# Optimization experiments

Measured on AMD Instinct MI355X. Metric: run time of the kernel, lower is better.

## Reference

```python
import jax, jax.numpy as jnp
import numpy as np

D_MODEL = 1024
N_HEADS = 16
D_HEAD = D_MODEL // N_HEADS


def setup_inputs() -> dict:
    key = jax.random.key(0)
    ks = jax.random.split(key, 5)
    scale = 1.0 / np.sqrt(D_MODEL)
    return {
        "x": jax.random.normal(ks[0], (2, 2048, D_MODEL), dtype=jnp.float32),
        "W_q": jax.random.normal(ks[1], (D_MODEL, D_MODEL), dtype=jnp.float32) * scale,
        "W_k": jax.random.normal(ks[2], (D_MODEL, D_MODEL), dtype=jnp.float32) * scale,
        "W_v": jax.random.normal(ks[3], (D_MODEL, D_MODEL), dtype=jnp.float32) * scale,
        "W_o": jax.random.normal(ks[4], (D_MODEL, D_MODEL), dtype=jnp.float32) * scale,
    }


def reference(x, W_q, W_k, W_v, W_o):
    B, S, _ = x.shape
    # nn.Linear computes x @ W.T; weights stored [out, in]
    def proj(W):
        y = jnp.einsum("bsd,ed->bse", x, W)
        return y.reshape(B, S, N_HEADS, D_HEAD).transpose(0, 2, 1, 3)  # [B,H,S,Dh]

    q, k, v = proj(W_q), proj(W_k), proj(W_v)
    scores = jnp.einsum("bhqd,bhkd->bhqk", q, k) / jnp.sqrt(jnp.float32(D_HEAD))
    causal = jnp.triu(jnp.ones((S, S), dtype=bool), k=1)
    scores = jnp.where(causal, -jnp.inf, scores)
    attn = jax.nn.softmax(scores, axis=-1)
    out = jnp.einsum("bhqk,bhkd->bhqd", attn, v)  # [B,H,S,Dh]
    out = out.transpose(0, 2, 1, 3).reshape(B, S, D_MODEL)
    return jnp.einsum("bsd,ed->bse", out, W_o)
```

## Files before the change

### kernel.cpp

```cpp
#include <hip/hip_runtime.h>


#define DMODEL 1024
#define NHEADS 16
#define DHEAD  64
#define SEQ    2048
#define BATCH  2
#define MROWS  (BATCH * SEQ)

typedef __bf16 bf16x8 __attribute__((ext_vector_type(8)));
typedef __bf16 bf16x4 __attribute__((ext_vector_type(4)));
typedef float  f32x4  __attribute__((ext_vector_type(4)));

__device__ __forceinline__ f32x4 mfma16(bf16x8 a, bf16x8 b, f32x4 c) {
    return __builtin_amdgcn_mfma_f32_16x16x32_bf16(a, b, c, 0, 0, 0);
}

__device__ __forceinline__ bf16x8 ld8(const float* p) {
    const f32x4 a0 = *(const f32x4*)p;
    const f32x4 a1 = *(const f32x4*)(p + 4);
    bf16x8 v;
    v[0] = (__bf16)a0[0]; v[1] = (__bf16)a0[1];
    v[2] = (__bf16)a0[2]; v[3] = (__bf16)a0[3];
    v[4] = (__bf16)a1[0]; v[5] = (__bf16)a1[1];
    v[6] = (__bf16)a1[2]; v[7] = (__bf16)a1[3];
    return v;
}

__device__ __forceinline__ void gll16(const __bf16* g, __bf16* l) {
    __builtin_amdgcn_global_load_lds(
        (const __attribute__((address_space(1))) void*)g,
        (__attribute__((address_space(3))) void*)l,
        16, 0, 0);
}

__global__ __launch_bounds__(256) void cvt_kernel(const float* __restrict__ x,
                                                  const float* __restrict__ Wq,
                                                  const float* __restrict__ Wk,
                                                  const float* __restrict__ Wv,
                                                  const float* __restrict__ Wo,
                                                  __bf16* __restrict__ xb,
                                                  __bf16* __restrict__ wcat) {
    const int y = blockIdx.y;
    const float* src;
    __bf16* dst;
    int nchunks;
    if (y == 0) { src = x; dst = xb; nchunks = (MROWS * DMODEL) / 8; }
    else {
        src = (y == 1) ? Wq : (y == 2) ? Wk : (y == 3) ? Wv : Wo;
        dst = wcat + (size_t)(y - 1) * DMODEL * DMODEL;
        nchunks = (DMODEL * DMODEL) / 8;
    }
    const int c = blockIdx.x * 256 + threadIdx.x;
    if (c < nchunks) *(bf16x8*)(dst + (size_t)c * 8) = ld8(src + (size_t)c * 8);
}

template <typename TC>
__device__ __forceinline__ void gemm_bb_body(const __bf16* __restrict__ A,
                                             const __bf16* __restrict__ W,
                                             TC* __restrict__ C,
                                             __bf16* __restrict__ VT,
                                             bool vt, int m0, int n0,
                                             float scale) {
    constexpr int K = DMODEL;
    __shared__ __align__(16) __bf16 As[128][32];
    __shared__ __align__(16) __bf16 Bs[128][32];

    const int tid  = threadIdx.x;
    const int lane = tid & 63;
    const int wave = tid >> 6;
    const int quad = lane >> 4;
    const int l16  = lane & 15;
    const int wm   = wave & 1;
    const int wn   = wave >> 1;

    const int srow = lane >> 2;
    const int scol = (lane & 3) * 8;

    const __bf16* a0p = A + (size_t)(m0 + wave * 16 + srow) * K + scol;
    const __bf16* a1p = A + (size_t)(m0 + 64 + wave * 16 + srow) * K + scol;
    const __bf16* b0p = W + (size_t)(n0 + wave * 16 + srow) * K + scol;
    const __bf16* b1p = W + (size_t)(n0 + 64 + wave * 16 + srow) * K + scol;

    f32x4 acc[4][4] = {};

    for (int k0 = 0; k0 < K; k0 += 32) {
        __syncthreads();
        gll16(a0p + k0, &As[wave * 16][0]);
        gll16(a1p + k0, &As[64 + wave * 16][0]);
        gll16(b0p + k0, &Bs[wave * 16][0]);
        gll16(b1p + k0, &Bs[64 + wave * 16][0]);
        __syncthreads();

        bf16x8 af[4], bfr[4];
#pragma unroll
        for (int i = 0; i < 4; ++i) {
            af[i]  = *(const bf16x8*)(&As[wm * 64 + i * 16 + l16][quad * 8]);
            bfr[i] = *(const bf16x8*)(&Bs[wn * 64 + i * 16 + l16][quad * 8]);
        }
#pragma unroll
        for (int mi = 0; mi < 4; ++mi)
#pragma unroll
            for (int ni = 0; ni < 4; ++ni)
                acc[mi][ni] = mfma16(af[mi], bfr[ni], acc[mi][ni]);
    }

    if (!vt) {
#pragma unroll
        for (int mi = 0; mi < 4; ++mi)
#pragma unroll
            for (int ni = 0; ni < 4; ++ni)
#pragma unroll
                for (int r = 0; r < 4; ++r) {
                    int row = m0 + wm * 64 + mi * 16 + quad * 4 + r;
                    int col = n0 + wn * 64 + ni * 16 + l16;
                    C[(size_t)row * DMODEL + col] = (TC)(acc[mi][ni][r] * scale);
                }
    } else {
#pragma unroll
        for (int mi = 0; mi < 4; ++mi)
#pragma unroll
            for (int ni = 0; ni < 4; ++ni) {
                const int m  = m0 + wm * 64 + mi * 16 + quad * 4;
                const int hd = n0 + wn * 64 + ni * 16 + l16;
                bf16x4 v4;
#pragma unroll
                for (int r = 0; r < 4; ++r) v4[r] = (__bf16)acc[mi][ni][r];
                *(bf16x4*)(VT + (size_t)hd * MROWS + m) = v4;
            }
    }
}

#define QSCALE 0.1803368801111204f

__global__ __launch_bounds__(256) void qkv_kernel(const __bf16* __restrict__ X,
                                                  const __bf16* __restrict__ wcat,
                                                  __bf16* __restrict__ Q,
                                                  __bf16* __restrict__ K,
                                                  __bf16* __restrict__ VT) {
    const int z = blockIdx.z;
    const __bf16* W = wcat + (size_t)z * DMODEL * DMODEL;
    __bf16* Y = (z == 0) ? Q : K;
    const float scale = (z == 0) ? QSCALE : 1.0f;
    gemm_bb_body<__bf16>(X, W, Y, VT, z == 2,
                         blockIdx.y * 128, blockIdx.x * 128, scale);
}

__global__ __launch_bounds__(256) void out_gemm_kernel(const __bf16* __restrict__ A,
                                                       const __bf16* __restrict__ W,
                                                       float* __restrict__ C) {
    gemm_bb_body<float>(A, W, C, nullptr, false,
                        blockIdx.y * 128, blockIdx.x * 128, 1.0f);
}

__global__ __launch_bounds__(256) void attn_kernel(const __bf16* __restrict__ Q,
                                                   const __bf16* __restrict__ Kg,
                                                   const __bf16* __restrict__ VTg,
                                                   __bf16* __restrict__ O) {
    const int bh  = blockIdx.x;
    const int y   = blockIdx.y;
    const int ya  = y >> 3, yr = y & 7;
    const int qt2 = (ya == 0) ? (31 - yr)
                  : (ya == 1) ? (16 + yr)
                  : (ya == 2) ? (15 - yr)
                  :             yr;
    const int b = bh >> 4, h = bh & 15;
    const size_t base = (size_t)b * SEQ * DMODEL + (size_t)h * DHEAD;

    const int tid  = threadIdx.x;
    const int lane = tid & 63;
    const int wave = tid >> 6;
    const int quad = lane >> 4;
    const int l16  = lane & 15;

    __shared__ __align__(16) __bf16 Ks[64][64];
    __shared__ __align__(16) __bf16 Vs[64][64];
    __shared__ __align__(16) __bf16 Ps[4][2][16][40];

    const int sr = lane >> 3;
    const int sc = ((lane & 7) ^ sr) * 8;

    const int qrow = qt2 * 64 + wave * 16 + l16;

    const bf16x8 qf0 = *(const bf16x8*)(Q + base + (size_t)qrow * DMODEL + quad * 8);
    const bf16x8 qf1 = *(const bf16x8*)(Q + base + (size_t)qrow * DMODEL + 32 + quad * 8);

    f32x4 oacc[4] = {};
    float m_i = -1e30f, l_i = 0.f;

    const int ntiles = qt2 + 1;
    const int gsw = (l16 & 7);

    for (int kt = 0; kt < ntiles; ++kt) {
        const int k0 = kt * 64;
        __syncthreads();
#pragma unroll
        for (int j = 0; j < 2; ++j) {
            const int row = wave * 16 + j * 8;
            gll16(Kg + base + (size_t)(k0 + row + sr) * DMODEL + sc, &Ks[row][0]);
            gll16(VTg + (size_t)(h * 64 + row + sr) * MROWS + (size_t)b * SEQ + k0 + sc,
                  &Vs[row][0]);
        }
        __syncthreads();

        const bool diag = (kt == ntiles - 1);

        f32x4 s[4];
#pragma unroll
        for (int g = 0; g < 4; ++g) {
            const bf16x8 kfa = *(const bf16x8*)(&Ks[g * 16 + l16][(quad ^ gsw) * 8]);
            const bf16x8 kfb = *(const bf16x8*)(&Ks[g * 16 + l16][((quad + 4) ^ gsw) * 8]);
            f32x4 t = {};
            t = mfma16(kfa, qf0, t);
            t = mfma16(kfb, qf1, t);
            s[g] = t;
        }

        float mx;
        bool ok[4][4];
        if (!diag) {
            mx = s[0][0];
#pragma unroll
            for (int g = 0; g < 4; ++g)
#pragma unroll
                for (int r = 0; r < 4; ++r) mx = fmaxf(mx, s[g][r]);
        } else {
            mx = -1e30f;
#pragma unroll
            for (int g = 0; g < 4; ++g)
#pragma unroll
                for (int r = 0; r < 4; ++r) {
                    const int kk = k0 + g * 16 + quad * 4 + r;
                    ok[g][r] = (kk <= qrow);
                    mx = fmaxf(mx, ok[g][r] ? s[g][r] : -1e30f);
                }
        }
        mx = fmaxf(mx, __shfl_xor(mx, 16));
        mx = fmaxf(mx, __shfl_xor(mx, 32));

        const bool defer = __all(mx - m_i <= 8.0f);
        float mnew;
        if (defer) {
            mnew = m_i;
        } else {
            mnew = fmaxf(m_i, mx);
            const float alpha = exp2f(m_i - mnew);
            m_i = mnew;
#pragma unroll
            for (int f = 0; f < 4; ++f) oacc[f] *= alpha;
            l_i *= alpha;
        }

        float rs = 0.f;
        bf16x4 w4[4];
        if (!diag) {
#pragma unroll
            for (int g = 0; g < 4; ++g)
#pragma unroll
                for (int r = 0; r < 4; ++r) {
                    const float p = exp2f(s[g][r] - mnew);
                    rs += p;
                    w4[g][r] = (__bf16)p;
                }
        } else {
#pragma unroll
            for (int g = 0; g < 4; ++g)
#pragma unroll
                for (int r = 0; r < 4; ++r) {
                    const float p = ok[g][r] ? exp2f(s[g][r] - mnew) : 0.f;
                    rs += p;
                    w4[g][r] = (__bf16)p;
                }
        }
        rs += __shfl_xor(rs, 16);
        rs += __shfl_xor(rs, 32);
        l_i += rs;

#pragma unroll
        for (int g = 0; g < 4; ++g)
            *(bf16x4*)(&Ps[wave][g >> 1][l16][(g & 1) * 16 + quad * 4]) = w4[g];

        const bf16x8 pf0 = *(const bf16x8*)(&Ps[wave][0][l16][quad * 8]);
        const bf16x8 pf1 = *(const bf16x8*)(&Ps[wave][1][l16][quad * 8]);
#pragma unroll
        for (int f = 0; f < 4; ++f) {
            const bf16x8 vfa = *(const bf16x8*)(&Vs[f * 16 + l16][(quad ^ gsw) * 8]);
            const bf16x8 vfb = *(const bf16x8*)(&Vs[f * 16 + l16][((quad + 4) ^ gsw) * 8]);
            f32x4 t = oacc[f];
            t = mfma16(vfa, pf0, t);
            t = mfma16(vfb, pf1, t);
            oacc[f] = t;
        }
    }

    const float inv = (l_i > 0.f) ? (1.f / l_i) : 0.f;
#pragma unroll
    for (int f = 0; f < 4; ++f) {
        bf16x4 o;
#pragma unroll
        for (int r = 0; r < 4; ++r) o[r] = (__bf16)(oacc[f][r] * inv);
        *(bf16x4*)(O + base + (size_t)qrow * DMODEL + f * 16 + quad * 4) = o;
    }
}

extern "C" void kernel_launch(void* const* d_in, const int* in_sizes, int n_in,
                              void* d_out, int out_size, void* d_ws, size_t ws_size,
                              hipStream_t stream) {
    const float* x  = (const float*)d_in[0];
    const float* Wq = (const float*)d_in[1];
    const float* Wk = (const float*)d_in[2];
    const float* Wv = (const float*)d_in[3];
    const float* Wo = (const float*)d_in[4];
    float* out = (float*)d_out;

    const size_t tm = (size_t)MROWS * DMODEL;
    const size_t tw = (size_t)DMODEL * DMODEL;
    __bf16* Q    = (__bf16*)d_ws;
    __bf16* K    = Q + tm;
    __bf16* VT   = K + tm;
    __bf16* xb   = VT + tm;
    __bf16* wcat = xb + tm;

    dim3 gc(2048, 5);
    cvt_kernel<<<gc, 256, 0, stream>>>(x, Wq, Wk, Wv, Wo, xb, wcat);

    dim3 g1(DMODEL / 128, MROWS / 128, 3);
    qkv_kernel<<<g1, 256, 0, stream>>>(xb, wcat, Q, K, VT);

    dim3 g2(BATCH * NHEADS, SEQ / 64);
    attn_kernel<<<g2, 256, 0, stream>>>(Q, K, VT, Q);

    dim3 g3(DMODEL / 128, MROWS / 128);
    out_gemm_kernel<<<g3, 256, 0, stream>>>(Q, wcat + 3 * tw, out);
}
```

Baseline: 187.1 us.

## Double-buffer K/V tiles in attention with async prefetch and MFMA priority

Splits the K and V shared-memory tiles into two buffers and prefetches the next tile with global-to-LDS loads while the current tile is computed. This leaves one barrier per iteration where there were two. It also wraps the MFMA sections in s_setprio raises and halves the P staging buffer by writing and reading it in two halves. Doubling the K/V buffers raises LDS use, which may lower occupancy. The reuse of the single P buffer relies on in-wave ordering being correct.

```diff
diff --git a/kernel.cpp b/kernel.cpp
--- a/kernel.cpp
+++ b/kernel.cpp
@@ -173,9 +173,9 @@
     const int quad = lane >> 4;
     const int l16  = lane & 15;
 
-    __shared__ __align__(16) __bf16 Ks[64][64];
-    __shared__ __align__(16) __bf16 Vs[64][64];
-    __shared__ __align__(16) __bf16 Ps[4][2][16][40];
+    __shared__ __align__(16) __bf16 Ks[2][64][64];
+    __shared__ __align__(16) __bf16 Vs[2][64][64];
+    __shared__ __align__(16) __bf16 Ps[4][16][40];
 
     const int sr = lane >> 3;
     const int sc = ((lane & 7) ^ sr) * 8;
@@ -185,36 +185,54 @@
     const bf16x8 qf0 = *(const bf16x8*)(Q + base + (size_t)qrow * DMODEL + quad * 8);
     const bf16x8 qf1 = *(const bf16x8*)(Q + base + (size_t)qrow * DMODEL + 32 + quad * 8);
 
+    const __bf16* kgp = Kg + base;
+    const __bf16* vgp = VTg + (size_t)(h * 64) * MROWS + (size_t)b * SEQ;
+
     f32x4 oacc[4] = {};
     float m_i = -1e30f, l_i = 0.f;
 
     const int ntiles = qt2 + 1;
     const int gsw = (l16 & 7);
 
+#pragma unroll
+    for (int j = 0; j < 2; ++j) {
+        const int row = wave * 16 + j * 8;
+        gll16(kgp + (size_t)(row + sr) * DMODEL + sc, &Ks[0][row][0]);
+        gll16(vgp + (size_t)(row + sr) * MROWS + sc, &Vs[0][row][0]);
+    }
+    asm volatile("s_waitcnt vmcnt(0)" ::: "memory");
+    __builtin_amdgcn_s_barrier();
+
+    int cur = 0;
     for (int kt = 0; kt < ntiles; ++kt) {
         const int k0 = kt * 64;
-        __syncthreads();
-#pragma unroll
-        for (int j = 0; j < 2; ++j) {
-            const int row = wave * 16 + j * 8;
-            gll16(Kg + base + (size_t)(k0 + row + sr) * DMODEL + sc, &Ks[row][0]);
-            gll16(VTg + (size_t)(h * 64 + row + sr) * MROWS + (size_t)b * SEQ + k0 + sc,
-                  &Vs[row][0]);
-        }
-        __syncthreads();
+
+        if (kt + 1 < ntiles) {
+            const int kn = k0 + 64;
+#pragma unroll
+            for (int j = 0; j < 2; ++j) {
+                const int row = wave * 16 + j * 8;
+                gll16(kgp + (size_t)(kn + row + sr) * DMODEL + sc,
+                      &Ks[cur ^ 1][row][0]);
+                gll16(vgp + (size_t)(row + sr) * MROWS + kn + sc,
+                      &Vs[cur ^ 1][row][0]);
+            }
+        }
 
         const bool diag = (kt == ntiles - 1);
 
         f32x4 s[4];
+        __builtin_amdgcn_s_setprio(1);
 #pragma unroll
         for (int g = 0; g < 4; ++g) {
-            const bf16x8 kfa = *(const bf16x8*)(&Ks[g * 16 + l16][(quad ^ gsw) * 8]);
-            const bf16x8 kfb = *(const bf16x8*)(&Ks[g * 16 + l16][((quad + 4) ^ gsw) * 8]);
+            const bf16x8 kfa = *(const bf16x8*)(&Ks[cur][g * 16 + l16][(quad ^ gsw) * 8]);
+            const bf16x8 kfb = *(const bf16x8*)(&Ks[cur][g * 16 + l16][((quad + 4) ^ gsw) * 8]);
             f32x4 t = {};
             t = mfma16(kfa, qf0, t);
             t = mfma16(kfb, qf1, t);
             s[g] = t;
         }
+        __builtin_amdgcn_s_setprio(0);
 
         float mx;
         bool ok[4][4];
@@ -276,21 +294,33 @@
         rs += __shfl_xor(rs, 32);
         l_i += rs;
 
-#pragma unroll
-        for (int g = 0; g < 4; ++g)
-            *(bf16x4*)(&Ps[wave][g >> 1][l16][(g & 1) * 16 + quad * 4]) = w4[g];
-
-        const bf16x8 pf0 = *(const bf16x8*)(&Ps[wave][0][l16][quad * 8]);
-        const bf16x8 pf1 = *(const bf16x8*)(&Ps[wave][1][l16][quad * 8]);
+        *(bf16x4*)(&Ps[wave][l16][quad * 4])      = w4[0];
+        *(bf16x4*)(&Ps[wave][l16][16 + quad * 4]) = w4[1];
+        const bf16x8 pf0 = *(const bf16x8*)(&Ps[wave][l16][quad * 8]);
+
+        __builtin_amdgcn_s_setprio(1);
 #pragma unroll
         for (int f = 0; f < 4; ++f) {
-            const bf16x8 vfa = *(const bf16x8*)(&Vs[f * 16 + l16][(quad ^ gsw) * 8]);
-            const bf16x8 vfb = *(const bf16x8*)(&Vs[f * 16 + l16][((quad + 4) ^ gsw) * 8]);
-            f32x4 t = oacc[f];
-            t = mfma16(vfa, pf0, t);
-            t = mfma16(vfb, pf1, t);
-            oacc[f] = t;
-        }
+            const bf16x8 vfa = *(const bf16x8*)(&Vs[cur][f * 16 + l16][(quad ^ gsw) * 8]);
+            oacc[f] = mfma16(vfa, pf0, oacc[f]);
+        }
+        __builtin_amdgcn_s_setprio(0);
+
+        *(bf16x4*)(&Ps[wave][l16][quad * 4])      = w4[2];
+        *(bf16x4*)(&Ps[wave][l16][16 + quad * 4]) = w4[3];
+        const bf16x8 pf1 = *(const bf16x8*)(&Ps[wave][l16][quad * 8]);
+
+        __builtin_amdgcn_s_setprio(1);
+#pragma unroll
+        for (int f = 0; f < 4; ++f) {
+            const bf16x8 vfb = *(const bf16x8*)(&Vs[cur][f * 16 + l16][((quad + 4) ^ gsw) * 8]);
+            oacc[f] = mfma16(vfb, pf1, oacc[f]);
+        }
+        __builtin_amdgcn_s_setprio(0);
+
+        asm volatile("s_waitcnt vmcnt(0)" ::: "memory");
+        __builtin_amdgcn_s_barrier();
+        cur ^= 1;
     }
 
     const float inv = (l_i > 0.f) ? (1.f / l_i) : 0.f;
```

Result: no change. 189.0 us (+1.0%).
